# Kernel optimization log

Measured on AMD Instinct MI355X. Metric: run time of the kernel, lower is better.

The kernel has to match this reference:

```python
import jax, jax.numpy as jnp
import numpy as np

EPS = 1e-5


def conv1x1(x, w, b=None):
    # x: [B,C,H,W], w: [O,C] (1x1 conv kernel squeezed)
    y = jnp.einsum('bchw,oc->bohw', x, w)
    if b is not None:
        y = y + b[None, :, None, None]
    return y


def bn_inf(x, g, b, m, v):
    scale = g / jnp.sqrt(v + EPS)
    return (x - m[None, :, None, None]) * scale[None, :, None, None] + b[None, :, None, None]


def setup_inputs() -> dict:
    B, C, H, W = 2, 256, 80, 80
    Ck, Cv, Co = 64, 128, 256
    key = jax.random.key(0)
    ks = jax.random.split(key, 16)
    d = {}
    d['x'] = jax.random.normal(ks[0], (B, C, H, W), dtype=jnp.float32)
    d['y'] = jax.random.normal(ks[1], (B, C, H, W), dtype=jnp.float32)
    s = 1.0 / np.sqrt(C)
    d['fk_w'] = jax.random.normal(ks[2], (Ck, C), dtype=jnp.float32) * s
    d['fk_g'] = jnp.ones((Ck,), jnp.float32)
    d['fk_b'] = jnp.zeros((Ck,), jnp.float32)
    d['fk_m'] = jax.random.normal(ks[3], (Ck,), dtype=jnp.float32) * 0.1
    d['fk_v'] = jax.random.uniform(ks[4], (Ck,), minval=0.5, maxval=1.5, dtype=jnp.float32)
    d['fq_w'] = jax.random.normal(ks[5], (Ck, C), dtype=jnp.float32) * s
    d['fq_g'] = jnp.ones((Ck,), jnp.float32)
    d['fq_b'] = jnp.zeros((Ck,), jnp.float32)
    d['fq_m'] = jax.random.normal(ks[6], (Ck,), dtype=jnp.float32) * 0.1
    d['fq_v'] = jax.random.uniform(ks[7], (Ck,), minval=0.5, maxval=1.5, dtype=jnp.float32)
    d['fv_w'] = jax.random.normal(ks[8], (Cv, C), dtype=jnp.float32) * s
    d['fv_b'] = jnp.zeros((Cv,), jnp.float32)
    d['W_w'] = jax.random.normal(ks[9], (Co, Cv), dtype=jnp.float32) * (1.0 / np.sqrt(Cv))
    d['W_b'] = jnp.zeros((Co,), jnp.float32)
    d['gamma'] = jnp.array([0.5], jnp.float32)
    return d


def reference(x, y, fk_w, fk_g, fk_b, fk_m, fk_v, fq_w, fq_g, fq_b, fq_m, fq_v, fv_w, fv_b, W_w, W_b, gamma):
    B, C, H, W = x.shape
    Ck = fk_w.shape[0]
    Cv = fv_w.shape[0]
    N = H * W
    # key from x, query/value from y (1x1 conv + BN projections)
    k = bn_inf(conv1x1(x, fk_w), fk_g, fk_b, fk_m, fk_v).reshape(B, Ck, N)          # [B,Ck,N]
    q = bn_inf(conv1x1(y, fq_w), fq_g, fq_b, fq_m, fq_v).reshape(B, Ck, N)          # [B,Ck,N]
    v = conv1x1(y, fv_w, fv_b).reshape(B, Cv, N)                                     # [B,Cv,N]
    sim = jnp.einsum('bkn,bkm->bnm', q, k) * (Ck ** -0.5)                            # [B,N,N]
    sim = jax.nn.softmax(sim, axis=-1)
    ctx = jnp.einsum('bnm,bvm->bvn', sim, v).reshape(B, Cv, H, W)                    # [B,Cv,H,W]
    ctx = conv1x1(ctx, W_w, W_b)                                                     # [B,Co,H,W]
    return gamma[0] * ctx + x
```

## Files before the change

### kernel.cpp

```cpp
#include <hip/hip_runtime.h>
#include <math.h>

#define NB   2
#define CIN  256
#define NN   6400
#define CKd  64
#define CVd  128
#define COd  256

using bf16   = __bf16;
using bf16x4 = __attribute__((ext_vector_type(4))) bf16;
using bf16x8 = __attribute__((ext_vector_type(8))) bf16;
using f32x4  = __attribute__((ext_vector_type(4))) float;

__device__ __forceinline__ void lds_cp16(const void* g, void* l) {
    __builtin_amdgcn_global_load_lds((const __attribute__((address_space(1))) void*)g,
                                     (__attribute__((address_space(3))) void*)l, 16, 0, 0);
}

__launch_bounds__(256, 4)
__global__ void projkqv_kernel(const float* __restrict__ x, const float* __restrict__ y,
                               const float* __restrict__ fk_w, const float* __restrict__ fk_g,
                               const float* __restrict__ fk_b, const float* __restrict__ fk_m,
                               const float* __restrict__ fk_v,
                               const float* __restrict__ fq_w, const float* __restrict__ fq_g,
                               const float* __restrict__ fq_b, const float* __restrict__ fq_m,
                               const float* __restrict__ fq_v,
                               const float* __restrict__ fv_w, const float* __restrict__ fv_b,
                               bf16* __restrict__ kb, bf16* __restrict__ qb, bf16* __restrict__ vb)
{
    __shared__ __align__(16) bf16 sbuf[64 * 128];
    __shared__ __align__(16) bf16 wbuf[64 * 128];

    const int tid  = threadIdx.x;
    const int lane = tid & 63, wav = tid >> 6;
    const int l15  = lane & 15, quad = lane >> 4;
    const int b    = blockIdx.z, m = blockIdx.y;
    const int n0   = blockIdx.x * 64;
    const float QS = 0.125f;

    const float* srcg = ((m == 0) ? x : y) + (size_t)b * CIN * NN;

    const int key = l15 & 7;
    f32x4 acc[4];
#pragma unroll
    for (int j = 0; j < 4; ++j) acc[j] = (f32x4){0.f, 0.f, 0.f, 0.f};

    for (int p = 0; p < 2; ++p) {
        if (p) __syncthreads();

        {
            const int r4  = lane >> 4;
            const int c16 = lane & 15;
#pragma unroll
            for (int i = 0; i < 4; ++i) {
                const int r  = wav * 16 + i * 4 + r4;
                const int cs = c16 ^ (r & 7);
                const float* ws = (m == 0) ? (fk_w + (size_t)r * CIN)
                                : (m == 1) ? (fq_w + (size_t)r * CIN)
                                : (fv_w + (size_t)((m - 2) * 64 + r) * CIN);
                const float4 w0 = *(const float4*)(ws + p * 128 + cs * 8);
                const float4 w1 = *(const float4*)(ws + p * 128 + cs * 8 + 4);
                float a = 1.0f;
                if (m == 0)      a = fk_g[r] * rsqrtf(fk_v[r] + 1e-5f);
                else if (m == 1) a = fq_g[r] * rsqrtf(fq_v[r] + 1e-5f) * QS;
                bf16x8 pk;
                pk[0] = (bf16)(w0.x * a); pk[1] = (bf16)(w0.y * a);
                pk[2] = (bf16)(w0.z * a); pk[3] = (bf16)(w0.w * a);
                pk[4] = (bf16)(w1.x * a); pk[5] = (bf16)(w1.y * a);
                pk[6] = (bf16)(w1.z * a); pk[7] = (bf16)(w1.w * a);
                *(bf16x8*)&wbuf[r * 128 + c16 * 8] = pk;
            }
        }
        {
            const int nl = (tid & 15) * 4;
            const int cq = tid >> 4;
            const int cb = p * 128 + cq * 8;
            float4 v[8];
#pragma unroll
            for (int e = 0; e < 8; ++e)
                v[e] = *(const float4*)(srcg + (size_t)(cb + e) * NN + n0 + nl);
#pragma unroll
            for (int i = 0; i < 4; ++i) {
                const int n = nl + i;
                bf16x8 pk;
#pragma unroll
                for (int e = 0; e < 8; ++e) pk[e] = (bf16)(&v[e].x)[i];
                *(bf16x8*)&sbuf[n * 128 + ((cq ^ (n & 7)) * 8)] = pk;
            }
        }
        __syncthreads();

        if (m < 2) {
            const int arow = wav * 16 + l15;
#pragma unroll
            for (int k4 = 0; k4 < 16; k4 += 4) {
                const bf16x8 af = *(const bf16x8*)&sbuf[arow * 128 + (((k4 + quad) ^ key) * 8)];
#pragma unroll
                for (int nt = 0; nt < 4; ++nt) {
                    const int brow = nt * 16 + l15;
                    const bf16x8 bfw = *(const bf16x8*)&wbuf[brow * 128 + (((k4 + quad) ^ key) * 8)];
                    acc[nt] = __builtin_amdgcn_mfma_f32_16x16x32_bf16(af, bfw, acc[nt], 0, 0, 0);
                }
            }
        } else {
            const int arow = wav * 16 + l15;
#pragma unroll
            for (int k4 = 0; k4 < 16; k4 += 4) {
                const bf16x8 af = *(const bf16x8*)&wbuf[arow * 128 + (((k4 + quad) ^ key) * 8)];
#pragma unroll
                for (int nt = 0; nt < 4; ++nt) {
                    const int brow = nt * 16 + l15;
                    const bf16x8 bfy = *(const bf16x8*)&sbuf[brow * 128 + (((k4 + quad) ^ key) * 8)];
                    acc[nt] = __builtin_amdgcn_mfma_f32_16x16x32_bf16(af, bfy, acc[nt], 0, 0, 0);
                }
            }
        }
    }

    if (m < 2) {
        bf16* dst = (m == 0) ? kb : qb;
        const int nb = n0 + wav * 16;
#pragma unroll
        for (int nt = 0; nt < 4; ++nt) {
            float bv;
            {
                const int c = nt * 16 + l15;
                if (m == 0) {
                    const float a = fk_g[c] * rsqrtf(fk_v[c] + 1e-5f);
                    bv = fk_b[c] - fk_m[c] * a;
                } else {
                    const float a = fq_g[c] * rsqrtf(fq_v[c] + 1e-5f);
                    bv = (fq_b[c] - fq_m[c] * a) * QS;
                }
            }
#pragma unroll
            for (int r = 0; r < 4; ++r) {
                const int n = nb + quad * 4 + r;
                dst[((size_t)b * NN + n) * CKd + nt * 16 + l15] = (bf16)(acc[nt][r] + bv);
            }
        }
    } else {
        const int cv0 = (m - 2) * 64 + wav * 16;
#pragma unroll
        for (int r = 0; r < 4; ++r) {
            const int cv = cv0 + quad * 4 + r;
            const float bv = fv_b[cv];
#pragma unroll
            for (int nt = 0; nt < 4; ++nt)
                vb[((size_t)b * CVd + cv) * NN + n0 + nt * 16 + l15] = (bf16)(acc[nt][r] + bv);
        }
    }
}

__launch_bounds__(256, 4)
__global__ void attn_kernel(const bf16* __restrict__ qb, const bf16* __restrict__ kb,
                            const bf16* __restrict__ vb,
                            bf16* __restrict__ pO, float* __restrict__ pl, int KS)
{
    __shared__ __align__(16) bf16 kbuf[2][64 * 64];
    __shared__ __align__(16) bf16 vbuf[128 * 64];
    __shared__ __align__(16) bf16 p_lds[4][16][64];

    const int lane = threadIdx.x & 63;
    const int wav  = threadIdx.x >> 6;
    const int l15  = lane & 15;
    const int quad = lane >> 4;
    const int r8   = lane >> 3;
    const int c_src = (lane & 7) ^ r8;
    const int sw   = l15 & 7;
    const int pkey = (l15 & 7) << 1;

    const int id    = blockIdx.x;
    const int ks    = id % KS;
    const int rst   = id / KS;
    const int b     = rst & 1;
    const int qtile = rst >> 1;
    const int q0    = qtile * 64 + wav * 16;

    const bf16* qrow = qb + (size_t)b * NN * CKd;
    const bf16* krow = kb + (size_t)b * NN * CKd;
    const bf16* vrow = vb + (size_t)b * CVd * NN;

    bf16x8 qf[2];
#pragma unroll
    for (int s = 0; s < 2; ++s)
        qf[s] = *(const bf16x8*)(qrow + (size_t)(q0 + l15) * CKd + s * 32 + quad * 8);

    const float ZC = -8.0f;
    const f32x4 zini = (f32x4){ZC, ZC, ZC, ZC};

    f32x4 acc[8];
#pragma unroll
    for (int cv = 0; cv < 8; ++cv) acc[cv] = (f32x4){0.f, 0.f, 0.f, 0.f};
    float psum = 0.f;

    const int t0 = (100 * ks) / KS;
    const int nt = (100 * (ks + 1)) / KS - t0;

    auto stageK = [&](int t, int bi) {
        const int key0 = t * 64;
        lds_cp16(krow + (size_t)(key0 + wav * 8 + r8) * CKd + c_src * 8,
                 &kbuf[bi][(wav * 8) * 64]);
        lds_cp16(krow + (size_t)(key0 + (wav + 4) * 8 + r8) * CKd + c_src * 8,
                 &kbuf[bi][((wav + 4) * 8) * 64]);
    };
    auto stageV = [&](int t) {
        const int key0 = t * 64;
#pragma unroll
        for (int g4 = 0; g4 < 4; ++g4) {
            const int g = wav * 4 + g4;
            lds_cp16(vrow + (size_t)(g * 8 + r8) * NN + key0 + c_src * 8,
                     &vbuf[(g * 8) * 64]);
        }
    };

    stageK(t0, 0);
    stageV(t0);
    __syncthreads();

    for (int t = 0; t < nt; ++t) {
        if (t + 1 < nt) stageK(t0 + t + 1, (t + 1) & 1);
        const bf16* kcur = &kbuf[t & 1][0];

        f32x4 s4[4];
#pragma unroll
        for (int kt = 0; kt < 4; ++kt) {
            const int rr = kt * 16 + l15;
            const bf16x8 kf0 = *(const bf16x8*)&kcur[rr * 64 + ((quad ^ sw) * 8)];
            const bf16x8 kf1 = *(const bf16x8*)&kcur[rr * 64 + (((4 + quad) ^ sw) * 8)];
            f32x4 z = zini;
            z = __builtin_amdgcn_mfma_f32_16x16x32_bf16(kf0, qf[0], z, 0, 0, 0);
            z = __builtin_amdgcn_mfma_f32_16x16x32_bf16(kf1, qf[1], z, 0, 0, 0);
            s4[kt] = z;
        }

#pragma unroll
        for (int kt = 0; kt < 4; ++kt) {
            bf16x4 pk;
#pragma unroll
            for (int r = 0; r < 4; ++r) {
                const float p = __expf(s4[kt][r]);
                psum += p;
                pk[r] = (bf16)p;
            }
            *(bf16x4*)&p_lds[wav][l15][((kt * 4 + quad) ^ pkey) * 4] = pk;
        }

        if (t + 1 < nt) { asm volatile("s_waitcnt vmcnt(2)" ::: "memory"); }
        else            { asm volatile("s_waitcnt vmcnt(0)" ::: "memory"); }
        __builtin_amdgcn_s_barrier();

        __builtin_amdgcn_s_setprio(1);
#pragma unroll
        for (int sp = 0; sp < 2; ++sp) {
            const bf16x8 pf = *(const bf16x8*)&p_lds[wav][l15][((sp * 8 + quad * 2) ^ pkey) * 4];
#pragma unroll
            for (int cvt = 0; cvt < 8; ++cvt) {
                const int rr = cvt * 16 + l15;
                const bf16x8 vf = *(const bf16x8*)&vbuf[rr * 64 + (((sp * 4 + quad) ^ sw) * 8)];
                acc[cvt] = __builtin_amdgcn_mfma_f32_16x16x32_bf16(vf, pf, acc[cvt], 0, 0, 0);
            }
        }
        __builtin_amdgcn_s_setprio(0);

        __syncthreads();
        if (t + 1 < nt) stageV(t0 + t + 1);
    }

    psum += __shfl_xor(psum, 16);
    psum += __shfl_xor(psum, 32);
    bf16* tbuf = &vbuf[wav * 2048];
    const size_t pb = (size_t)ks * NB + b;
#pragma unroll
    for (int cvt = 0; cvt < 8; ++cvt) {
        bf16x4 pk;
#pragma unroll
        for (int r = 0; r < 4; ++r) pk[r] = (bf16)acc[cvt][r];
        const int u = (cvt * 4 + quad) ^ (l15 << 1);
        *(bf16x4*)&tbuf[l15 * 128 + u * 4] = pk;
    }
#pragma unroll
    for (int j = 0; j < 4; ++j) {
        const int row = j * 4 + (lane >> 4);
        const int g   = ((lane & 15) * 2) ^ ((row & 15) << 1);
        const bf16x8 vv = *(const bf16x8*)&tbuf[row * 128 + g * 4];
        *(bf16x8*)(pO + (pb * NN + q0) * CVd + j * 512 + lane * 8) = vv;
    }
    if (quad == 0) pl[pb * NN + q0 + l15] = psum;
}

__launch_bounds__(256, 4)
__global__ void outproj_kernel(const bf16* __restrict__ pO, const float* __restrict__ pl,
                               const float* __restrict__ W_w, const float* __restrict__ W_b,
                               const float* __restrict__ x, const float* __restrict__ gam,
                               float* __restrict__ out, int KS)
{
    __shared__ __align__(16) bf16 wbuf[128 * 128];
    __shared__ __align__(16) bf16 cbuf[32 * 128];

    const int tid  = threadIdx.x;
    const int lane = tid & 63, wav = tid >> 6;
    const int l15  = lane & 15, quad = lane >> 4;
    const int b    = blockIdx.y;
    const int n0   = blockIdx.x * 32;

    auto stage_w = [&](int p) {
        const int r4 = lane >> 4;
        const int c16 = lane & 15;
#pragma unroll
        for (int i = 0; i < 8; ++i) {
            const int r  = wav * 32 + i * 4 + r4;
            const int cs = c16 ^ (r & 7);
            const float* ws = W_w + (size_t)(p * 128 + r) * CVd + cs * 8;
            const float4 w0 = *(const float4*)(ws);
            const float4 w1 = *(const float4*)(ws + 4);
            bf16x8 pk;
            pk[0] = (bf16)w0.x; pk[1] = (bf16)w0.y; pk[2] = (bf16)w0.z; pk[3] = (bf16)w0.w;
            pk[4] = (bf16)w1.x; pk[5] = (bf16)w1.y; pk[6] = (bf16)w1.z; pk[7] = (bf16)w1.w;
            *(bf16x8*)&wbuf[r * 128 + c16 * 8] = pk;
        }
    };
    stage_w(0);

    const int tn = tid >> 3;
    const int tc = (tid & 7) * 16;
    const size_t kstr = (size_t)NB * NN * CVd;
    const bf16* src0 = pO + ((size_t)b * NN + n0 + tn) * CVd + tc;
    float vacc[16];
#pragma unroll
    for (int i = 0; i < 16; ++i) vacc[i] = 0.f;
    float L = 0.f;

    bf16x8 c0 = *(const bf16x8*)(src0);
    bf16x8 c1 = *(const bf16x8*)(src0 + 8);
    for (int ksi = 0; ksi < KS; ++ksi) {
        bf16x8 nx0 = c0, nx1 = c1;
        if (ksi + 1 < KS) {
            const bf16* s = src0 + (size_t)(ksi + 1) * kstr;
            nx0 = *(const bf16x8*)(s);
            nx1 = *(const bf16x8*)(s + 8);
        }
        L += pl[(size_t)(ksi * NB + b) * NN + n0 + tn];
#pragma unroll
        for (int e = 0; e < 8; ++e) vacc[e]     += (float)c0[e];
#pragma unroll
        for (int e = 0; e < 8; ++e) vacc[8 + e] += (float)c1[e];
        c0 = nx0; c1 = nx1;
    }
    {
        const float rL = 1.0f / L;
#pragma unroll
        for (int j = 0; j < 2; ++j) {
            bf16x8 o;
#pragma unroll
            for (int e = 0; e < 8; ++e) o[e] = (bf16)(vacc[j * 8 + e] * rL);
            const int c = (tid & 7) * 2 + j;
            *(bf16x8*)&cbuf[tn * 128 + ((c ^ (tn & 7)) * 8)] = o;
        }
    }
    __syncthreads();

    const float gm = gam[0];

    auto mfma_pass = [&](f32x4 (&acc)[2][2]) {
#pragma unroll
        for (int i = 0; i < 2; ++i)
#pragma unroll
            for (int j = 0; j < 2; ++j) acc[i][j] = (f32x4){0.f, 0.f, 0.f, 0.f};
#pragma unroll
        for (int kk = 0; kk < 4; ++kk) {
#pragma unroll
            for (int cot = 0; cot < 2; ++cot) {
                const int arow = wav * 32 + cot * 16 + l15;
                const bf16x8 af = *(const bf16x8*)&wbuf[arow * 128 + (((kk * 4 + quad) ^ (arow & 7)) * 8)];
#pragma unroll
                for (int nt = 0; nt < 2; ++nt) {
                    const int brow = nt * 16 + l15;
                    const bf16x8 bfc = *(const bf16x8*)&cbuf[brow * 128 + (((kk * 4 + quad) ^ (brow & 7)) * 8)];
                    acc[cot][nt] = __builtin_amdgcn_mfma_f32_16x16x32_bf16(af, bfc, acc[cot][nt], 0, 0, 0);
                }
            }
        }
    };
    auto store_pass = [&](const f32x4 (&acc)[2][2], int p) {
#pragma unroll
        for (int cot = 0; cot < 2; ++cot)
#pragma unroll
            for (int r = 0; r < 4; ++r) {
                const int co = p * 128 + wav * 32 + cot * 16 + quad * 4 + r;
                const float bv = W_b[co];
#pragma unroll
                for (int nt = 0; nt < 2; ++nt) {
                    const int n = n0 + nt * 16 + l15;
                    const size_t a = ((size_t)b * COd + co) * NN + n;
                    out[a] = gm * (acc[cot][nt][r] + bv) + x[a];
                }
            }
    };

    f32x4 acc0[2][2];
    mfma_pass(acc0);
    __syncthreads();
    stage_w(1);
    store_pass(acc0, 0);
    __syncthreads();
    f32x4 acc1[2][2];
    mfma_pass(acc1);
    store_pass(acc1, 1);
}

extern "C" void kernel_launch(void* const* d_in, const int* in_sizes, int n_in,
                              void* d_out, int out_size, void* d_ws, size_t ws_size,
                              hipStream_t stream)
{
    const float* x     = (const float*)d_in[0];
    const float* y     = (const float*)d_in[1];
    const float* fk_w  = (const float*)d_in[2];
    const float* fk_g  = (const float*)d_in[3];
    const float* fk_b  = (const float*)d_in[4];
    const float* fk_m  = (const float*)d_in[5];
    const float* fk_v  = (const float*)d_in[6];
    const float* fq_w  = (const float*)d_in[7];
    const float* fq_g  = (const float*)d_in[8];
    const float* fq_b  = (const float*)d_in[9];
    const float* fq_m  = (const float*)d_in[10];
    const float* fq_v  = (const float*)d_in[11];
    const float* fv_w  = (const float*)d_in[12];
    const float* fv_b  = (const float*)d_in[13];
    const float* W_w   = (const float*)d_in[14];
    const float* W_b   = (const float*)d_in[15];
    const float* gamma = (const float*)d_in[16];
    float* out = (float*)d_out;

    char* ws = (char*)d_ws;
    size_t off = 0;
    auto carve = [&](size_t bytes) -> char* {
        char* p = ws + off;
        off = (off + bytes + 255) & ~(size_t)255;
        return p;
    };

    bf16*  kb   = (bf16*)carve((size_t)NB * NN * CKd * 2);
    bf16*  qbuf = (bf16*)carve((size_t)NB * NN * CKd * 2);
    bf16*  vb   = (bf16*)carve((size_t)NB * CVd * NN * 2);

    const size_t region = ws_size - off;
    const size_t per_ks = (size_t)NB * NN * CVd * 2 + (size_t)NB * NN * 4 + 512;
    int KS = 1;
    {
        const int cand[4] = {5, 4, 2, 1};
        for (int i = 0; i < 4; ++i)
            if ((size_t)cand[i] * per_ks <= region) { KS = cand[i]; break; }
    }
    bf16*  pO = (bf16*)carve((size_t)KS * NB * NN * CVd * 2);
    float* pl = (float*)carve((size_t)KS * NB * NN * 4);

    const dim3 blk(256);
    projkqv_kernel<<<dim3(100, 4, NB), blk, 0, stream>>>(x, y,
                                                         fk_w, fk_g, fk_b, fk_m, fk_v,
                                                         fq_w, fq_g, fq_b, fq_m, fq_v,
                                                         fv_w, fv_b, kb, qbuf, vb);
    attn_kernel<<<dim3(100 * NB * KS), blk, 0, stream>>>(qbuf, kb, vb, pO, pl, KS);
    outproj_kernel<<<dim3(200, NB), blk, 0, stream>>>(pO, pl, W_w, W_b, x, gamma, out, KS);
}
```

Before: 161.1 us.

## Process two query tiles per wave in attention to reuse K/V tiles

Each wave in the attention kernel now handles 32 query rows (two 16-row tiles) instead of 16, and the attention grid is halved. Each K and V fragment read from shared memory then feeds twice as many MFMAs, cutting LDS and global staging traffic per unit of work. The P scratch buffer doubles and is also reused for the output transpose. The cost is higher register pressure (launch bounds lowered to 3 blocks) and fewer blocks to spread across the CUs.

```diff
diff --git a/kernel.cpp b/kernel.cpp
--- a/kernel.cpp
+++ b/kernel.cpp
@@ -153,14 +153,14 @@
     }
 }
 
-__launch_bounds__(256, 4)
+__launch_bounds__(256, 3)
 __global__ void attn_kernel(const bf16* __restrict__ qb, const bf16* __restrict__ kb,
                             const bf16* __restrict__ vb,
                             bf16* __restrict__ pO, float* __restrict__ pl, int KS)
 {
     __shared__ __align__(16) bf16 kbuf[2][64 * 64];
     __shared__ __align__(16) bf16 vbuf[128 * 64];
-    __shared__ __align__(16) bf16 p_lds[4][16][64];
+    __shared__ __align__(16) bf16 p_lds[4][2][16][64];
 
     const int lane = threadIdx.x & 63;
     const int wav  = threadIdx.x >> 6;
@@ -176,24 +176,28 @@
     const int rst   = id / KS;
     const int b     = rst & 1;
     const int qtile = rst >> 1;
-    const int q0    = qtile * 64 + wav * 16;
+    const int q0    = qtile * 128 + wav * 32;
 
     const bf16* qrow = qb + (size_t)b * NN * CKd;
     const bf16* krow = kb + (size_t)b * NN * CKd;
     const bf16* vrow = vb + (size_t)b * CVd * NN;
 
-    bf16x8 qf[2];
-#pragma unroll
-    for (int s = 0; s < 2; ++s)
-        qf[s] = *(const bf16x8*)(qrow + (size_t)(q0 + l15) * CKd + s * 32 + quad * 8);
+    bf16x8 qf[2][2];
+#pragma unroll
+    for (int qtl = 0; qtl < 2; ++qtl)
+#pragma unroll
+        for (int s = 0; s < 2; ++s)
+            qf[qtl][s] = *(const bf16x8*)(qrow + (size_t)(q0 + qtl * 16 + l15) * CKd + s * 32 + quad * 8);
 
     const float ZC = -8.0f;
     const f32x4 zini = (f32x4){ZC, ZC, ZC, ZC};
 
-    f32x4 acc[8];
-#pragma unroll
-    for (int cv = 0; cv < 8; ++cv) acc[cv] = (f32x4){0.f, 0.f, 0.f, 0.f};
-    float psum = 0.f;
+    f32x4 acc[2][8];
+#pragma unroll
+    for (int qtl = 0; qtl < 2; ++qtl)
+#pragma unroll
+        for (int cv = 0; cv < 8; ++cv) acc[qtl][cv] = (f32x4){0.f, 0.f, 0.f, 0.f};
+    float psum[2] = {0.f, 0.f};
 
     const int t0 = (100 * ks) / KS;
     const int nt = (100 * (ks + 1)) / KS - t0;
@@ -223,28 +227,36 @@
         if (t + 1 < nt) stageK(t0 + t + 1, (t + 1) & 1);
         const bf16* kcur = &kbuf[t & 1][0];
 
-        f32x4 s4[4];
+        f32x4 s4[2][4];
 #pragma unroll
         for (int kt = 0; kt < 4; ++kt) {
             const int rr = kt * 16 + l15;
             const bf16x8 kf0 = *(const bf16x8*)&kcur[rr * 64 + ((quad ^ sw) * 8)];
             const bf16x8 kf1 = *(const bf16x8*)&kcur[rr * 64 + (((4 + quad) ^ sw) * 8)];
-            f32x4 z = zini;
-            z = __builtin_amdgcn_mfma_f32_16x16x32_bf16(kf0, qf[0], z, 0, 0, 0);
-            z = __builtin_amdgcn_mfma_f32_16x16x32_bf16(kf1, qf[1], z, 0, 0, 0);
-            s4[kt] = z;
-        }
-
-#pragma unroll
-        for (int kt = 0; kt < 4; ++kt) {
-            bf16x4 pk;
-#pragma unroll
-            for (int r = 0; r < 4; ++r) {
-                const float p = __expf(s4[kt][r]);
-                psum += p;
-                pk[r] = (bf16)p;
-            }
-            *(bf16x4*)&p_lds[wav][l15][((kt * 4 + quad) ^ pkey) * 4] = pk;
+#pragma unroll
+            for (int qtl = 0; qtl < 2; ++qtl) {
+                f32x4 z = zini;
+                z = __builtin_amdgcn_mfma_f32_16x16x32_bf16(kf0, qf[qtl][0], z, 0, 0, 0);
+                z = __builtin_amdgcn_mfma_f32_16x16x32_bf16(kf1, qf[qtl][1], z, 0, 0, 0);
+                s4[qtl][kt] = z;
+            }
+        }
+
+#pragma unroll
+        for (int qtl = 0; qtl < 2; ++qtl) {
+            float ps = 0.f;
+#pragma unroll
+            for (int kt = 0; kt < 4; ++kt) {
+                bf16x4 pk;
+#pragma unroll
+                for (int r = 0; r < 4; ++r) {
+                    const float p = __expf(s4[qtl][kt][r]);
+                    ps += p;
+                    pk[r] = (bf16)p;
+                }
+                *(bf16x4*)&p_lds[wav][qtl][l15][((kt * 4 + quad) ^ pkey) * 4] = pk;
+            }
+            psum[qtl] += ps;
         }
 
         if (t + 1 < nt) { asm volatile("s_waitcnt vmcnt(2)" ::: "memory"); }
@@ -254,12 +266,14 @@
         __builtin_amdgcn_s_setprio(1);
 #pragma unroll
         for (int sp = 0; sp < 2; ++sp) {
-            const bf16x8 pf = *(const bf16x8*)&p_lds[wav][l15][((sp * 8 + quad * 2) ^ pkey) * 4];
+            const bf16x8 pf0 = *(const bf16x8*)&p_lds[wav][0][l15][((sp * 8 + quad * 2) ^ pkey) * 4];
+            const bf16x8 pf1 = *(const bf16x8*)&p_lds[wav][1][l15][((sp * 8 + quad * 2) ^ pkey) * 4];
 #pragma unroll
             for (int cvt = 0; cvt < 8; ++cvt) {
                 const int rr = cvt * 16 + l15;
                 const bf16x8 vf = *(const bf16x8*)&vbuf[rr * 64 + (((sp * 4 + quad) ^ sw) * 8)];
-                acc[cvt] = __builtin_amdgcn_mfma_f32_16x16x32_bf16(vf, pf, acc[cvt], 0, 0, 0);
+                acc[0][cvt] = __builtin_amdgcn_mfma_f32_16x16x32_bf16(vf, pf0, acc[0][cvt], 0, 0, 0);
+                acc[1][cvt] = __builtin_amdgcn_mfma_f32_16x16x32_bf16(vf, pf1, acc[1][cvt], 0, 0, 0);
             }
         }
         __builtin_amdgcn_s_setprio(0);
@@ -268,26 +282,30 @@
         if (t + 1 < nt) stageV(t0 + t + 1);
     }
 
-    psum += __shfl_xor(psum, 16);
-    psum += __shfl_xor(psum, 32);
-    bf16* tbuf = &vbuf[wav * 2048];
+    __syncthreads();
+    bf16* tbuf = &p_lds[wav][0][0][0];
     const size_t pb = (size_t)ks * NB + b;
 #pragma unroll
-    for (int cvt = 0; cvt < 8; ++cvt) {
-        bf16x4 pk;
-#pragma unroll
-        for (int r = 0; r < 4; ++r) pk[r] = (bf16)acc[cvt][r];
-        const int u = (cvt * 4 + quad) ^ (l15 << 1);
-        *(bf16x4*)&tbuf[l15 * 128 + u * 4] = pk;
-    }
-#pragma unroll
-    for (int j = 0; j < 4; ++j) {
-        const int row = j * 4 + (lane >> 4);
-        const int g   = ((lane & 15) * 2) ^ ((row & 15) << 1);
-        const bf16x8 vv = *(const bf16x8*)&tbuf[row * 128 + g * 4];
-        *(bf16x8*)(pO + (pb * NN + q0) * CVd + j * 512 + lane * 8) = vv;
-    }
-    if (quad == 0) pl[pb * NN + q0 + l15] = psum;
+    for (int qt = 0; qt < 2; ++qt) {
+        psum[qt] += __shfl_xor(psum[qt], 16);
+        psum[qt] += __shfl_xor(psum[qt], 32);
+#pragma unroll
+        for (int cvt = 0; cvt < 8; ++cvt) {
+            bf16x4 pk;
+#pragma unroll
+            for (int r = 0; r < 4; ++r) pk[r] = (bf16)acc[qt][cvt][r];
+            const int u = (cvt * 4 + quad) ^ (l15 << 1);
+            *(bf16x4*)&tbuf[l15 * 128 + u * 4] = pk;
+        }
+#pragma unroll
+        for (int j = 0; j < 4; ++j) {
+            const int row = j * 4 + (lane >> 4);
+            const int g   = ((lane & 15) * 2) ^ ((row & 15) << 1);
+            const bf16x8 vv = *(const bf16x8*)&tbuf[row * 128 + g * 4];
+            *(bf16x8*)(pO + (pb * NN + q0 + qt * 16) * CVd + j * 512 + lane * 8) = vv;
+        }
+        if (quad == 0) pl[pb * NN + q0 + qt * 16 + l15] = psum[qt];
+    }
 }
 
 __launch_bounds__(256, 4)
@@ -461,6 +479,6 @@
                                                          fk_w, fk_g, fk_b, fk_m, fk_v,
                                                          fq_w, fq_g, fq_b, fq_m, fq_v,
                                                          fv_w, fv_b, kb, qbuf, vb);
-    attn_kernel<<<dim3(100 * NB * KS), blk, 0, stream>>>(qbuf, kb, vb, pO, pl, KS);
+    attn_kernel<<<dim3(50 * NB * KS), blk, 0, stream>>>(qbuf, kb, vb, pO, pl, KS);
     outproj_kernel<<<dim3(200, NB), blk, 0, stream>>>(pO, pl, W_w, W_b, x, gamma, out, KS);
 }
```

Measured after the change: 162.0 us. About the same (+0.6%).
